# Performance work log

Hardware: AMD Instinct MI355X
Metric: run time of the kernel (lower is better)

## Reference

```python
import jax, jax.numpy as jnp
import numpy as np
import math

# ---- config (matches init_kwargs / Mamba defaults) ----
B_SZ = 16
IMG = 224
PATCH = 16
D_MODEL = 384
DEPTH = 24
D_INNER = 2 * D_MODEL          # expand=2
D_STATE = 16
D_CONV = 4
DT_RANK = math.ceil(D_MODEL / D_STATE)
N_CLASSES = 1000
L_TOK = (IMG // PATCH) ** 2     # 196

C_CURV = 0.5
SQRT_C = math.sqrt(C_CURV)
MAX_NORM = 0.95 / SQRT_C

# ---- StablePoincareBall ops ----
def _norm(x):
    return jnp.sqrt(jnp.sum(x * x, axis=-1, keepdims=True) + 1e-15)

def expmap0(u):
    n = jnp.clip(_norm(u), 1e-8, 5.0)
    res = jnp.tanh(SQRT_C * n) / SQRT_C * (u / n)
    rn = _norm(res)
    scale = jnp.where(rn > MAX_NORM, MAX_NORM / rn, jnp.ones_like(rn))
    return res * scale

def logmap0(y):
    n = jnp.clip(_norm(y), 1e-8, MAX_NORM)
    return jnp.arctanh(jnp.minimum(SQRT_C * n, 0.95)) / SQRT_C * (y / n)

def mobius_add(a, b):
    xy = jnp.sum(a * b, -1, keepdims=True)
    x2 = jnp.sum(a * a, -1, keepdims=True)
    y2 = jnp.sum(b * b, -1, keepdims=True)
    num = (1 + 2 * C_CURV * xy + C_CURV * y2) * a + (1 - C_CURV * x2) * b
    den = 1 + 2 * C_CURV * xy + (C_CURV ** 2) * x2 * y2
    return num / jnp.maximum(den, 1e-15)

def mobius_matvec(M, x):
    xn = jnp.maximum(_norm(x), 1e-8)
    mx = x @ M.T
    mxn = jnp.maximum(_norm(mx), 1e-8)
    t = jnp.tanh(mxn / xn * jnp.arctanh(jnp.minimum(SQRT_C * xn, 1.0 - 1e-5)))
    return t * mx / (mxn * SQRT_C)

def hyp_layernorm(x, gamma, beta, eps=1e-5):
    t = logmap0(x)
    mean = t.mean(-1, keepdims=True)
    # torch .std() is unbiased (ddof=1)
    var = jnp.sum((t - mean) ** 2, -1, keepdims=True) / (t.shape[-1] - 1)
    tn = (t - mean) / (jnp.sqrt(var) + eps)
    return expmap0(tn * gamma + beta)

def silu(x):
    return x * jax.nn.sigmoid(x)

# ---- Mamba selective scan (recompute dA per step; carry only h) ----
def selective_scan(u, dt, A, Bm, Cm):
    # u, dt: (B,L,Din); A: (Din,N); Bm, Cm: (B,L,N)
    def step(h, inp):
        dt_t, B_t, C_t, u_t = inp              # (B,Din),(B,N),(B,N),(B,Din)
        dA = jnp.exp(dt_t[..., None] * A)      # (B,Din,N)
        h = dA * h + dt_t[..., None] * B_t[:, None, :] * u_t[..., None]
        y = jnp.sum(h * C_t[:, None, :], -1)   # (B,Din)
        return h, y
    h0 = jnp.zeros((u.shape[0], u.shape[2], A.shape[1]), u.dtype)
    _, ys = jax.lax.scan(step, h0, (dt.transpose(1, 0, 2), Bm.transpose(1, 0, 2),
                                    Cm.transpose(1, 0, 2), u.transpose(1, 0, 2)))
    return ys.transpose(1, 0, 2)               # (B,L,Din)

def mamba_mixer(x, in_w, cw, cb, xp_w, dt_w, dt_b, A_log, Dp, out_w):
    xz = x @ in_w.T                            # (B,L,2*Din)
    xc, z = xz[..., :D_INNER], xz[..., D_INNER:]
    xt = xc.transpose(0, 2, 1)                 # (B,Din,L)
    xpad = jnp.pad(xt, ((0, 0), (0, 0), (D_CONV - 1, 0)))
    L = xt.shape[-1]
    conv = sum(cw[:, k][None, :, None] * xpad[:, :, k:k + L] for k in range(D_CONV))
    conv = conv + cb[None, :, None]
    u = silu(conv.transpose(0, 2, 1))          # (B,L,Din)
    dbl = u @ xp_w.T                           # (B,L,dt_rank+2N)
    dt_r = dbl[..., :DT_RANK]
    Bm = dbl[..., DT_RANK:DT_RANK + D_STATE]
    Cm = dbl[..., DT_RANK + D_STATE:]
    dt = jax.nn.softplus(dt_r @ dt_w.T + dt_b)
    A = -jnp.exp(A_log)
    y = selective_scan(u, dt, A, Bm, Cm) + Dp * u
    y = y * silu(z)
    return y @ out_w.T


def setup_inputs() -> dict:
    key = jax.random.key(0)
    ks = jax.random.split(key, 24)
    f32 = jnp.float32
    inp = {}
    inp['x'] = jax.random.normal(ks[0], (B_SZ, 3, IMG, IMG), f32)
    inp['patch_w'] = jax.random.normal(ks[1], (D_MODEL, 3, PATCH, PATCH), f32) * 0.02
    inp['patch_b'] = jax.random.normal(ks[2], (D_MODEL,), f32) * 0.005
    inp['hyp_w'] = jax.random.normal(ks[3], (D_MODEL, D_MODEL), f32) * (1.0 / math.sqrt(D_MODEL))
    inp['hyp_b'] = jax.random.normal(ks[4], (D_MODEL,), f32) * 0.01
    inp['pe_gamma'] = jnp.ones((D_MODEL,), f32)
    inp['pe_beta'] = jnp.zeros((D_MODEL,), f32)
    inp['pos_embed'] = jax.random.normal(ks[5], (1, L_TOK, D_MODEL), f32) * 0.02
    inp['in_proj_w'] = jax.random.normal(ks[6], (DEPTH, 2 * D_INNER, D_MODEL), f32) * 0.02
    inp['conv_w'] = jax.random.normal(ks[7], (DEPTH, D_INNER, D_CONV), f32) * 0.1
    inp['conv_b'] = jnp.zeros((DEPTH, D_INNER), f32)
    inp['x_proj_w'] = jax.random.normal(ks[8], (DEPTH, DT_RANK + 2 * D_STATE, D_INNER), f32) * 0.02
    inp['dt_proj_w'] = jax.random.normal(ks[9], (DEPTH, D_INNER, DT_RANK), f32) * (1.0 / math.sqrt(DT_RANK))
    inp['dt_proj_b'] = jnp.log(jnp.expm1(jnp.full((DEPTH, D_INNER), 0.01, f32)))  # dt init ~0.01
    inp['A_log'] = jnp.tile(jnp.log(jnp.arange(1, D_STATE + 1, dtype=f32))[None, None, :], (DEPTH, D_INNER, 1))
    inp['Dp'] = jnp.ones((DEPTH, D_INNER), f32)
    inp['out_proj_w'] = jax.random.normal(ks[10], (DEPTH, D_MODEL, D_INNER), f32) * (0.02 / math.sqrt(DEPTH))
    inp['gamma'] = jnp.ones((DEPTH, D_MODEL), f32)
    inp['beta'] = jnp.zeros((DEPTH, D_MODEL), f32)
    inp['gamma_f'] = jnp.ones((D_MODEL,), f32)
    inp['beta_f'] = jnp.zeros((D_MODEL,), f32)
    inp['prototypes'] = expmap0(jax.random.normal(ks[11], (N_CLASSES, D_MODEL), f32) * 0.1)
    return inp


def reference(x, patch_w, patch_b, hyp_w, hyp_b, pe_gamma, pe_beta, pos_embed,
              in_proj_w, conv_w, conv_b, x_proj_w, dt_proj_w, dt_proj_b,
              A_log, Dp, out_proj_w, gamma, beta, gamma_f, beta_f, prototypes):
    # patch embed conv
    feat = jax.lax.conv_general_dilated(x, patch_w, (PATCH, PATCH), 'VALID',
                                        dimension_numbers=('NCHW', 'OIHW', 'NCHW'))
    feat = feat + patch_b[None, :, None, None]
    B, D, Hp, Wp = feat.shape
    tokens = feat.reshape(B, D, Hp * Wp).transpose(0, 2, 1)   # (B,L,D)
    h = expmap0(tokens)
    h = mobius_add(mobius_matvec(hyp_w, h), hyp_b)
    h = hyp_layernorm(h, pe_gamma, pe_beta)
    h = expmap0(logmap0(h) + pos_embed)                        # tangent-space pos add
    hidden, residual = h, None
    for i in range(DEPTH):
        residual = hidden if residual is None else hidden + residual
        hn = hyp_layernorm(residual, gamma[i], beta[i])
        hidden = mamba_mixer(hn, in_proj_w[i], conv_w[i], conv_b[i], x_proj_w[i],
                             dt_proj_w[i], dt_proj_b[i], A_log[i], Dp[i], out_proj_w[i])
    residual = hidden + residual
    hf = hyp_layernorm(residual, gamma_f, beta_f)
    pooled = expmap0(logmap0(hf).mean(axis=1))                 # tangent mean pool
    # hyperbolic distance head: logits = -dist(x, prototypes)
    diff = mobius_add(-pooled[:, None, :], prototypes[None])
    dn = jnp.minimum(SQRT_C * _norm(diff)[..., 0], 1.0 - 1e-5)
    return -(2.0 / SQRT_C) * jnp.arctanh(dn)                   # (B, num_classes)
```

## Files before the change

### kernel.cpp

```cpp
#include <hip/hip_runtime.h>
#include <hip/hip_bf16.h>
#include <math.h>

#define D_MODEL 384
#define D_INNER 768
#define D_STATE 16
#define DT_RANK 24
#define NXP 56
#define LTOK 196
#define BSZ 16
#define NROW 3136
#define NDEPTH 24
#define NCLS 1000

constexpr float kSqrtC   = 0.70710678118654752440f;
constexpr float kMaxNorm = 0.95f / 0.70710678118654752440f;

typedef unsigned short u16;
typedef short  bf16x8 __attribute__((ext_vector_type(8)));
typedef u16    u16x8  __attribute__((ext_vector_type(8)));
typedef float  f32x4  __attribute__((ext_vector_type(4)));

__device__ __forceinline__ float clampf(float x, float lo, float hi) {
  return fminf(fmaxf(x, lo), hi);
}

__device__ __forceinline__ u16 f2bf(float f) {
  union { float f; unsigned u; } v; v.f = f;
  return (u16)((v.u + 0x7FFFu + ((v.u >> 16) & 1u)) >> 16);
}
__device__ __forceinline__ float bf2f(u16 s) {
  union { unsigned u; float f; } v; v.u = ((unsigned)s) << 16;
  return v.f;
}

__device__ __forceinline__ float fsig(float x) {
  return __fdividef(1.f, 1.f + __expf(-x));
}
__device__ __forceinline__ float fsilu(float x) { return x * fsig(x); }
__device__ __forceinline__ float fsoftplus(float x) {
  return (x > 20.f) ? x : __logf(1.f + __expf(x));
}
__device__ __forceinline__ float ftanh(float x) {
  float e = __expf(2.f * x);
  return __fdividef(e - 1.f, e + 1.f);
}
__device__ __forceinline__ float fatanh(float x) {
  return 0.5f * __logf(__fdividef(1.f + x, 1.f - x));
}

__device__ __forceinline__ float waveSum(float v) {
#pragma unroll
  for (int o = 1; o < 64; o <<= 1) v += __shfl_xor(v, o, 64);
  return v;
}

__device__ __forceinline__ float blockSum128(float v, float* sm) {
#pragma unroll
  for (int o = 32; o > 0; o >>= 1) v += __shfl_down(v, o, 64);
  __syncthreads();
  if ((threadIdx.x & 63) == 0) sm[threadIdx.x >> 6] = v;
  __syncthreads();
  return sm[0] + sm[1];
}

__global__ __launch_bounds__(256) void k_cvt(const float* __restrict__ s,
                                             u16* __restrict__ d, int n4) {
  int i = blockIdx.x * 256 + threadIdx.x;
  if (i >= n4) return;
  float4 v = ((const float4*)s)[i];
  short4 o = {(short)f2bf(v.x), (short)f2bf(v.y), (short)f2bf(v.z),
              (short)f2bf(v.w)};
  *(short4*)&d[(size_t)i * 4] = o;
}

__global__ __launch_bounds__(256) void k_im2col(const float* __restrict__ x,
                                                u16* __restrict__ P) {
  size_t idx = (size_t)blockIdx.x * 256 + threadIdx.x;
  if (idx >= (size_t)NROW * 768) return;
  int k = (int)(idx % 768);
  int r = (int)(idx / 768);
  int b = r / LTOK, t = r % LTOK;
  int hp = t / 14, wp = t % 14;
  int c = k / 256, rem = k % 256, i = rem / 16, j = rem % 16;
  P[idx] = f2bf(
      x[(((size_t)(b * 3 + c) * 224) + hp * 16 + i) * 224 + wp * 16 + j]);
}

#define LDA 40
__global__ __launch_bounds__(256) void k_gemm_bb(
    const u16* __restrict__ A, const u16* __restrict__ W,
    const float* __restrict__ bias, void* __restrict__ Cn,
    void* __restrict__ Ct, int K, int lda, int ldc, int ldct, int Nv, int act,
    int obf, int obf_t) {
  __shared__ u16 As[64 * LDA];
  __shared__ u16 Ws[64 * LDA];
  const int tid = threadIdx.x;
  const int m0 = blockIdx.x * 64;
  const int n0 = blockIdx.y * 64;
  const int lane = tid & 63;
  const int wave = tid >> 6;
  const int wm = wave & 1, wn = wave >> 1;
  const int lm = lane & 15;
  const int quad = lane >> 4;
  const int srow = tid >> 2;
  const int sseg = tid & 3;

  f32x4 acc[2][2];
#pragma unroll
  for (int i = 0; i < 2; i++)
#pragma unroll
    for (int j = 0; j < 2; j++) acc[i][j] = (f32x4){0.f, 0.f, 0.f, 0.f};

  const u16* rowA = A + (size_t)(m0 + srow) * lda + sseg * 8;
  const int wrow = n0 + srow;
  const u16* rowW = W + (size_t)wrow * K + sseg * 8;
  const bool wvalid = wrow < Nv;

  for (int k0 = 0; k0 < K; k0 += 32) {
    u16x8 av = {0, 0, 0, 0, 0, 0, 0, 0}, wv = {0, 0, 0, 0, 0, 0, 0, 0};
    if (k0 + 32 <= K) {
      av = *(const u16x8*)(rowA + k0);
      if (wvalid) wv = *(const u16x8*)(rowW + k0);
    } else {
#pragma unroll
      for (int kk = 0; kk < 8; kk++) {
        int k = k0 + sseg * 8 + kk;
        if (k < K) {
          av[kk] = rowA[k0 + kk];
          if (wvalid) wv[kk] = rowW[k0 + kk];
        }
      }
    }
    __syncthreads();
    *(u16x8*)&As[srow * LDA + sseg * 8] = av;
    *(u16x8*)&Ws[srow * LDA + sseg * 8] = wv;
    __syncthreads();
    bf16x8 af[2], bfr[2];
#pragma unroll
    for (int i = 0; i < 2; i++) {
      af[i]  = *(bf16x8*)&As[(wm * 32 + i * 16 + lm) * LDA + quad * 8];
      bfr[i] = *(bf16x8*)&Ws[(wn * 32 + i * 16 + lm) * LDA + quad * 8];
    }
#pragma unroll
    for (int i = 0; i < 2; i++)
#pragma unroll
      for (int j = 0; j < 2; j++)
        acc[i][j] = __builtin_amdgcn_mfma_f32_16x16x32_bf16(af[i], bfr[j],
                                                            acc[i][j], 0, 0, 0);
  }
#pragma unroll
  for (int i = 0; i < 2; i++) {
#pragma unroll
    for (int j = 0; j < 2; j++) {
      int cg = n0 + wn * 32 + j * 16 + lm;
      if (cg >= Nv) continue;
      float bj = bias ? bias[cg] : 0.f;
      float o[4];
      int rgb = m0 + wm * 32 + i * 16 + quad * 4;
#pragma unroll
      for (int reg = 0; reg < 4; reg++) {
        float v = acc[i][j][reg] + bj;
        if (act == 1) v = fsoftplus(v);
        else if (act == 2 && cg >= 768) v = fsilu(v);
        o[reg] = v;
      }
      if (Cn) {
#pragma unroll
        for (int reg = 0; reg < 4; reg++) {
          if (obf) ((u16*)Cn)[(size_t)(rgb + reg) * ldc + cg] = f2bf(o[reg]);
          else ((float*)Cn)[(size_t)(rgb + reg) * ldc + cg] = o[reg];
        }
      }
      if (Ct) {
        if (obf_t) {
          short4 o4 = {(short)f2bf(o[0]), (short)f2bf(o[1]), (short)f2bf(o[2]),
                       (short)f2bf(o[3])};
          *(short4*)&((u16*)Ct)[(size_t)cg * ldct + rgb] = o4;
        } else {
          float4 o4 = {o[0], o[1], o[2], o[3]};
          *(float4*)&((float*)Ct)[(size_t)cg * ldct + rgb] = o4;
        }
      }
    }
  }
}

__global__ __launch_bounds__(256) void k_gemm_n128(
    const u16* __restrict__ A, const u16* __restrict__ W,
    const float* __restrict__ bias, void* __restrict__ Cn, int K, int lda,
    int ldc, int act, int obf) {
  __shared__ u16 As[64 * LDA];
  __shared__ u16 Ws[128 * LDA];
  const int tid = threadIdx.x;
  const int m0 = blockIdx.x * 64;
  const int n0 = blockIdx.y * 128;
  const int lane = tid & 63;
  const int w = tid >> 6;
  const int lm = lane & 15;
  const int quad = lane >> 4;
  const int srow = tid >> 2;
  const int sseg = tid & 3;
  const int wrow = tid >> 1;
  const int wseg = tid & 1;

  f32x4 acc[4][2];
#pragma unroll
  for (int i = 0; i < 4; i++)
#pragma unroll
    for (int j = 0; j < 2; j++) acc[i][j] = (f32x4){0.f, 0.f, 0.f, 0.f};

  const u16* rowA = A + (size_t)(m0 + srow) * lda + sseg * 8;
  const u16* rowW = W + (size_t)(n0 + wrow) * K + wseg * 16;

  for (int k0 = 0; k0 < K; k0 += 32) {
    u16x8 av = *(const u16x8*)(rowA + k0);
    u16x8 wv0 = *(const u16x8*)(rowW + k0);
    u16x8 wv1 = *(const u16x8*)(rowW + k0 + 8);
    __syncthreads();
    *(u16x8*)&As[srow * LDA + sseg * 8] = av;
    *(u16x8*)&Ws[wrow * LDA + wseg * 16] = wv0;
    *(u16x8*)&Ws[wrow * LDA + wseg * 16 + 8] = wv1;
    __syncthreads();
    bf16x8 af[4], bfr[2];
#pragma unroll
    for (int i = 0; i < 4; i++)
      af[i] = *(bf16x8*)&As[(i * 16 + lm) * LDA + quad * 8];
#pragma unroll
    for (int j = 0; j < 2; j++)
      bfr[j] = *(bf16x8*)&Ws[(w * 32 + j * 16 + lm) * LDA + quad * 8];
#pragma unroll
    for (int i = 0; i < 4; i++)
#pragma unroll
      for (int j = 0; j < 2; j++)
        acc[i][j] = __builtin_amdgcn_mfma_f32_16x16x32_bf16(af[i], bfr[j],
                                                            acc[i][j], 0, 0, 0);
  }
#pragma unroll
  for (int i = 0; i < 4; i++) {
#pragma unroll
    for (int j = 0; j < 2; j++) {
      int cg = n0 + w * 32 + j * 16 + lm;
      float bj = bias ? bias[cg] : 0.f;
      int rgb = m0 + i * 16 + quad * 4;
#pragma unroll
      for (int reg = 0; reg < 4; reg++) {
        float v = acc[i][j][reg] + bj;
        if (act == 1) v = fsoftplus(v);
        else if (act == 2 && cg >= 768) v = fsilu(v);
        if (obf) ((u16*)Cn)[(size_t)(rgb + reg) * ldc + cg] = f2bf(v);
        else ((float*)Cn)[(size_t)(rgb + reg) * ldc + cg] = v;
      }
    }
  }
}

__global__ __launch_bounds__(128) void k_stem_a(const float* __restrict__ tok,
                                                u16* __restrict__ hb,
                                                float* __restrict__ xn) {
  __shared__ float sm[2];
  const int r = blockIdx.x, tid = threadIdx.x;
  float v[3];
#pragma unroll
  for (int j = 0; j < 3; j++) v[j] = tok[(size_t)r * D_MODEL + tid + j * 128];
  float s = blockSum128(v[0] * v[0] + v[1] * v[1] + v[2] * v[2], sm);
  float n = sqrtf(s + 1e-15f);
  float nc = clampf(n, 1e-8f, 5.f);
  float ke = tanhf(kSqrtC * nc) / (kSqrtC * nc);
  float rn = sqrtf(ke * ke * s + 1e-15f);
  float sc = rn > kMaxNorm ? kMaxNorm / rn : 1.f;
  float kk = ke * sc;
#pragma unroll
  for (int j = 0; j < 3; j++)
    hb[(size_t)r * D_MODEL + tid + j * 128] = f2bf(kk * v[j]);
  if (tid == 0) xn[r] = fmaxf(sqrtf(kk * kk * s + 1e-15f), 1e-8f);
}

__global__ __launch_bounds__(128) void k_stem_b(
    const float* __restrict__ mx, const float* __restrict__ xn,
    const float* __restrict__ hyp_b, const float* __restrict__ pe_g,
    const float* __restrict__ pe_b, const float* __restrict__ pos,
    float* __restrict__ outh) {
  __shared__ float sm[2];
  const int r = blockIdx.x, tid = threadIdx.x;
  const int t = r % LTOK;
  float mv[3], bv[3];
  int dd[3];
#pragma unroll
  for (int j = 0; j < 3; j++) {
    dd[j] = tid + j * 128;
    mv[j] = mx[(size_t)r * D_MODEL + dd[j]];
    bv[j] = hyp_b[dd[j]];
  }
  float smx = blockSum128(mv[0] * mv[0] + mv[1] * mv[1] + mv[2] * mv[2], sm);
  float mxn = fmaxf(sqrtf(smx + 1e-15f), 1e-8f);
  float xnv = xn[r];
  float tt = tanhf(mxn / xnv * atanhf(fminf(kSqrtC * xnv, 1.f - 1e-5f)));
  float kres = tt / (mxn * kSqrtC);
  float res[3];
#pragma unroll
  for (int j = 0; j < 3; j++) res[j] = kres * mv[j];
  float xy = blockSum128(res[0] * bv[0] + res[1] * bv[1] + res[2] * bv[2], sm);
  float y2 = blockSum128(bv[0] * bv[0] + bv[1] * bv[1] + bv[2] * bv[2], sm);
  float x2 = kres * kres * smx;
  float al = 1.f + xy + 0.5f * y2;
  float be = 1.f - 0.5f * x2;
  float den = fmaxf(1.f + xy + 0.25f * x2 * y2, 1e-15f);
  float h1[3];
#pragma unroll
  for (int j = 0; j < 3; j++) h1[j] = (al * res[j] + be * bv[j]) / den;
  float s1 = blockSum128(h1[0] * h1[0] + h1[1] * h1[1] + h1[2] * h1[2], sm);
  float n1 = sqrtf(s1 + 1e-15f);
  float nc1 = clampf(n1, 1e-8f, kMaxNorm);
  float kl = atanhf(fminf(kSqrtC * nc1, 0.95f)) / (kSqrtC * nc1);
  float tl[3];
#pragma unroll
  for (int j = 0; j < 3; j++) tl[j] = kl * h1[j];
  float mean = blockSum128(tl[0] + tl[1] + tl[2], sm) * (1.f / 384.f);
  float dv = 0.f;
#pragma unroll
  for (int j = 0; j < 3; j++) { float d = tl[j] - mean; dv += d * d; }
  float var = blockSum128(dv, sm) * (1.f / 383.f);
  float inv = 1.f / (sqrtf(var) + 1e-5f);
  float g[3];
#pragma unroll
  for (int j = 0; j < 3; j++)
    g[j] = (tl[j] - mean) * inv * pe_g[dd[j]] + pe_b[dd[j]];
  float sg = blockSum128(g[0] * g[0] + g[1] * g[1] + g[2] * g[2], sm);
  float ng = sqrtf(sg + 1e-15f);
  float nc2 = clampf(ng, 1e-8f, 5.f);
  float ke = tanhf(kSqrtC * nc2) / (kSqrtC * nc2);
  float rn = sqrtf(ke * ke * sg + 1e-15f);
  float sc = rn > kMaxNorm ? kMaxNorm / rn : 1.f;
  float kk = ke * sc;
  float s2 = kk * kk * sg;
  float n3 = sqrtf(s2 + 1e-15f);
  float nc3 = clampf(n3, 1e-8f, kMaxNorm);
  float kl2 = atanhf(fminf(kSqrtC * nc3, 0.95f)) / (kSqrtC * nc3);
  float v[3];
#pragma unroll
  for (int j = 0; j < 3; j++)
    v[j] = kl2 * kk * g[j] + pos[(size_t)t * D_MODEL + dd[j]];
  float sv = blockSum128(v[0] * v[0] + v[1] * v[1] + v[2] * v[2], sm);
  float nv = sqrtf(sv + 1e-15f);
  float nc4 = clampf(nv, 1e-8f, 5.f);
  float ke2 = tanhf(kSqrtC * nc4) / (kSqrtC * nc4);
  float rn2 = sqrtf(ke2 * ke2 * sv + 1e-15f);
  float sc2 = rn2 > kMaxNorm ? kMaxNorm / rn2 : 1.f;
#pragma unroll
  for (int j = 0; j < 3; j++)
    outh[(size_t)r * D_MODEL + dd[j]] = ke2 * sc2 * v[j];
}

__global__ __launch_bounds__(256) void k_resln(
    const float* __restrict__ hid, const float* __restrict__ res_in,
    float* __restrict__ res_out, const float* __restrict__ g_,
    const float* __restrict__ b_, u16* __restrict__ out_bf,
    float* __restrict__ out_f, int first, int out_logmap) {
  const int lane = threadIdx.x & 63;
  const int r = blockIdx.x * 4 + (threadIdx.x >> 6);
  float v[6];
  int dd[6];
#pragma unroll
  for (int j = 0; j < 6; j++) {
    dd[j] = lane + j * 64;
    size_t idx = (size_t)r * D_MODEL + dd[j];
    v[j] = hid[idx] + (first ? 0.f : res_in[idx]);
    res_out[idx] = v[j];
  }
  float ss = 0.f;
#pragma unroll
  for (int j = 0; j < 6; j++) ss += v[j] * v[j];
  float s = waveSum(ss);
  float n = sqrtf(s + 1e-15f);
  float nc = clampf(n, 1e-8f, kMaxNorm);
  float kl = fatanh(fminf(kSqrtC * nc, 0.95f)) / (kSqrtC * nc);
  float t[6];
  float ts = 0.f;
#pragma unroll
  for (int j = 0; j < 6; j++) { t[j] = kl * v[j]; ts += t[j]; }
  float mean = waveSum(ts) * (1.f / 384.f);
  float dv = 0.f;
#pragma unroll
  for (int j = 0; j < 6; j++) { float d = t[j] - mean; dv += d * d; }
  float var = waveSum(dv) * (1.f / 383.f);
  float inv = 1.f / (sqrtf(var) + 1e-5f);
  float g[6];
  float gs = 0.f;
#pragma unroll
  for (int j = 0; j < 6; j++) {
    g[j] = (t[j] - mean) * inv * g_[dd[j]] + b_[dd[j]];
    gs += g[j] * g[j];
  }
  float sg = waveSum(gs);
  float ng = sqrtf(sg + 1e-15f);
  float nc2 = clampf(ng, 1e-8f, 5.f);
  float ke = ftanh(kSqrtC * nc2) / (kSqrtC * nc2);
  float rn = sqrtf(ke * ke * sg + 1e-15f);
  float sc = rn > kMaxNorm ? kMaxNorm / rn : 1.f;
  float kk = ke * sc;
  if (!out_logmap) {
#pragma unroll
    for (int j = 0; j < 6; j++)
      out_bf[(size_t)r * D_MODEL + dd[j]] = f2bf(kk * g[j]);
  } else {
    float s2 = kk * kk * sg;
    float n3 = sqrtf(s2 + 1e-15f);
    float nc3 = clampf(n3, 1e-8f, kMaxNorm);
    float kl2 = fatanh(fminf(kSqrtC * nc3, 0.95f)) / (kSqrtC * nc3);
#pragma unroll
    for (int j = 0; j < 6; j++)
      out_f[(size_t)r * D_MODEL + dd[j]] = kl2 * kk * g[j];
  }
}

__global__ __launch_bounds__(256) void k_convt(const u16* __restrict__ xz,
                                               const float* __restrict__ cw,
                                               const float* __restrict__ cb,
                                               u16* __restrict__ ut,
                                               u16* __restrict__ un) {
  __shared__ u16 sx[52][68];
  __shared__ u16 su2[49][68];
  const int d0 = blockIdx.x * 64;
  const int l0 = blockIdx.y * 49;
  const int b = blockIdx.z;
  const int t = threadIdx.x;
#pragma unroll
  for (int i = 0; i < 4; i++) {
    int idx = t + i * 256;
    if (idx < 832) {
      int row = idx >> 4, seg = idx & 15;
      int l = l0 - 3 + row;
      short4 v = {0, 0, 0, 0};
      if (l >= 0) {
        const u16* p = xz + (size_t)(b * LTOK + l) * (2 * D_INNER) + d0 + seg * 4;
        v = *(const short4*)p;
      }
      *(short4*)&sx[row][seg * 4] = v;
    }
  }
  __syncthreads();
  const int dl = t & 63, lg = t >> 6;
  const int d = d0 + dl;
  const float c0 = cw[d * 4], c1 = cw[d * 4 + 1], c2 = cw[d * 4 + 2],
              c3 = cw[d * 4 + 3];
  const float bb = cb[d];
  for (int l = lg; l < 49; l += 4) {
    float acc = bb;
    acc = fmaf(c0, bf2f(sx[l + 0][dl]), acc);
    acc = fmaf(c1, bf2f(sx[l + 1][dl]), acc);
    acc = fmaf(c2, bf2f(sx[l + 2][dl]), acc);
    acc = fmaf(c3, bf2f(sx[l + 3][dl]), acc);
    su2[l][dl] = f2bf(fsilu(acc));
  }
  __syncthreads();
#pragma unroll
  for (int i = 0; i < 13; i++) {
    int idx = t + i * 256;
    if (idx < 3136) {
      int d_ = idx / 49, l_ = idx % 49;
      ut[(size_t)(d0 + d_) * NROW + b * LTOK + l0 + l_] = su2[l_][d_];
    }
  }
#pragma unroll
  for (int i = 0; i < 13; i++) {
    int idx = t + i * 256;
    if (idx < 3136) {
      int l_ = idx >> 6, d_ = idx & 63;
      un[(size_t)(b * LTOK + l0 + l_) * D_INNER + d0 + d_] = su2[l_][d_];
    }
  }
}

__global__ __launch_bounds__(256) void k_pscan(
    const u16* __restrict__ ut, const float* __restrict__ dblt,
    const float* __restrict__ dt_w, const float* __restrict__ dt_bias,
    const float* __restrict__ A_log, const float* __restrict__ Dp,
    u16* __restrict__ yt) {
  __shared__ float sdt[4][196];
  __shared__ float su[4][196];
  __shared__ float sprod[16][197];
  const int d0 = blockIdx.x * 4, b = blockIdx.y;
  const int t = threadIdx.x;
  const size_t col0 = (size_t)b * LTOK;
  if (t < 196) {
    float r[DT_RANK];
#pragma unroll
    for (int k = 0; k < DT_RANK; k++)
      r[k] = dblt[(size_t)k * NROW + col0 + t];
#pragma unroll
    for (int g = 0; g < 4; g++) {
      const int d = d0 + g;
      float acc = dt_bias[d];
#pragma unroll
      for (int k = 0; k < DT_RANK; k++)
        acc = fmaf(r[k], dt_w[d * DT_RANK + k], acc);
      sdt[g][t] = fsoftplus(acc);
      su[g][t] = bf2f(ut[(size_t)d * NROW + col0 + t]);
    }
  }
  const int c = t & 15, n = t >> 4;
  const bool act = c < 14;
  float Breg[14], Creg[14];
  if (act) {
    const float2* Bp =
        (const float2*)(dblt + (size_t)(DT_RANK + n) * NROW + col0 + c * 14);
    const float2* Cp = (const float2*)(
        dblt + (size_t)(DT_RANK + D_STATE + n) * NROW + col0 + c * 14);
#pragma unroll
    for (int j = 0; j < 7; j++) {
      float2 bv = Bp[j], cv = Cp[j];
      Breg[2 * j] = bv.x; Breg[2 * j + 1] = bv.y;
      Creg[2 * j] = cv.x; Creg[2 * j + 1] = cv.y;
    }
  }
  __syncthreads();
  for (int g = 0; g < 4; g++) {
    const int d = d0 + g;
    const float a = -__expf(A_log[(size_t)d * D_STATE + n]);
    float dA[14], hh[14];
    float A = 1.f, Bc = 0.f;
    if (act) {
      float h = 0.f, p = 1.f;
#pragma unroll
      for (int j = 0; j < 14; j++) {
        int l = c * 14 + j;
        float dtv = sdt[g][l];
        float e = __expf(dtv * a);
        h = fmaf(e, h, dtv * Breg[j] * su[g][l]);
        dA[j] = e;
        hh[j] = h;
        p *= e;
      }
      A = p;
      Bc = h;
    }
#pragma unroll
    for (int off = 1; off < 16; off <<= 1) {
      float pA = __shfl_up(A, off, 16);
      float pB = __shfl_up(Bc, off, 16);
      if (c >= off) {
        Bc = fmaf(A, pB, Bc);
        A *= pA;
      }
    }
    float h0 = __shfl_up(Bc, 1, 16);
    if (c == 0) h0 = 0.f;
    if (act) {
      float p = 1.f;
#pragma unroll
      for (int j = 0; j < 14; j++) {
        p *= dA[j];
        sprod[n][c * 14 + j] = fmaf(p, h0, hh[j]) * Creg[j];
      }
    }
    __syncthreads();
    if (t < 196) {
      float y = 0.f;
#pragma unroll
      for (int nn = 0; nn < 16; nn++) y += sprod[nn][t];
      yt[(size_t)d * NROW + col0 + t] = f2bf(fmaf(Dp[d], su[g][t], y));
    }
    __syncthreads();
  }
}

__global__ __launch_bounds__(256) void k_trgate(const u16* __restrict__ yt,
                                                const u16* __restrict__ xz,
                                                u16* __restrict__ yf) {
  __shared__ u16 st[49][68];
  const int d0 = blockIdx.x * 64;
  const int l0 = blockIdx.y * 49;
  const int b = blockIdx.z;
  const int t = threadIdx.x;
#pragma unroll
  for (int i = 0; i < 13; i++) {
    int idx = t + i * 256;
    if (idx < 3136) {
      int d_ = idx / 49, l_ = idx % 49;
      st[l_][d_] = yt[(size_t)(d0 + d_) * NROW + b * LTOK + l0 + l_];
    }
  }
  __syncthreads();
#pragma unroll
  for (int i = 0; i < 13; i++) {
    int idx = t + i * 256;
    if (idx < 3136) {
      int l_ = idx >> 6, d_ = idx & 63;
      size_t r = (size_t)(b * LTOK + l0 + l_);
      float z = bf2f(xz[r * (2 * D_INNER) + D_INNER + d0 + d_]);
      yf[r * D_INNER + d0 + d_] = f2bf(bf2f(st[l_][d_]) * z);
    }
  }
}

__global__ __launch_bounds__(128) void k_pool1(const float* __restrict__ tl,
                                               float* __restrict__ partial) {
  const int b = blockIdx.x, g = blockIdx.y, tid = threadIdx.x;
  float m[3] = {0.f, 0.f, 0.f};
  for (int l = g * 14; l < (g + 1) * 14; l++) {
    size_t row = ((size_t)b * LTOK + l) * D_MODEL;
#pragma unroll
    for (int j = 0; j < 3; j++) m[j] += tl[row + tid + j * 128];
  }
#pragma unroll
  for (int j = 0; j < 3; j++)
    partial[((size_t)b * 14 + g) * D_MODEL + tid + j * 128] = m[j];
}

__global__ __launch_bounds__(128) void k_pool2(const float* __restrict__ partial,
                                               float* __restrict__ pooled,
                                               float* __restrict__ x2v) {
  __shared__ float sm[2];
  const int b = blockIdx.x, tid = threadIdx.x;
  float m[3] = {0.f, 0.f, 0.f};
  for (int g = 0; g < 14; g++) {
    size_t row = ((size_t)b * 14 + g) * D_MODEL;
#pragma unroll
    for (int j = 0; j < 3; j++) m[j] += partial[row + tid + j * 128];
  }
#pragma unroll
  for (int j = 0; j < 3; j++) m[j] *= (1.f / (float)LTOK);
  float s = blockSum128(m[0] * m[0] + m[1] * m[1] + m[2] * m[2], sm);
  float n = sqrtf(s + 1e-15f);
  float nc = clampf(n, 1e-8f, 5.f);
  float ke = tanhf(kSqrtC * nc) / (kSqrtC * nc);
  float rn = sqrtf(ke * ke * s + 1e-15f);
  float sc = rn > kMaxNorm ? kMaxNorm / rn : 1.f;
  float kk = ke * sc;
  float p[3];
#pragma unroll
  for (int j = 0; j < 3; j++) {
    p[j] = kk * m[j];
    pooled[(size_t)b * D_MODEL + tid + j * 128] = p[j];
  }
  float s2 = blockSum128(p[0] * p[0] + p[1] * p[1] + p[2] * p[2], sm);
  if (tid == 0) x2v[b] = s2;
}

__global__ __launch_bounds__(256) void k_head(const float* __restrict__ pooled,
                                              const float* __restrict__ protos,
                                              const float* __restrict__ x2v,
                                              float* __restrict__ out) {
  __shared__ float sp[D_MODEL];
  const int b = blockIdx.y;
  const int c = blockIdx.x * 256 + threadIdx.x;
  for (int j = threadIdx.x; j < D_MODEL; j += 256)
    sp[j] = pooled[(size_t)b * D_MODEL + j];
  __syncthreads();
  if (c >= NCLS) return;
  const float* pr = protos + (size_t)c * D_MODEL;
  float dotv = 0.f, y2 = 0.f;
  for (int k = 0; k < D_MODEL; k++) {
    float w = pr[k];
    dotv += sp[k] * w;
    y2 += w * w;
  }
  float x2 = x2v[b];
  float xy = -dotv;
  float al = 1.f + xy + 0.5f * y2;
  float be = 1.f - 0.5f * x2;
  float num2 = al * al * x2 + 2.f * al * be * xy + be * be * y2;
  float den = fmaxf(1.f + xy + 0.25f * x2 * y2, 1e-15f);
  float r2 = num2 / (den * den) + 1e-15f;
  float dn = fminf(kSqrtC * sqrtf(r2), 1.f - 1e-5f);
  out[(size_t)b * NCLS + c] = -(2.f / kSqrtC) * atanhf(dn);
}

extern "C" void kernel_launch(void* const* d_in, const int* in_sizes, int n_in,
                              void* d_out, int out_size, void* d_ws,
                              size_t ws_size, hipStream_t stream) {
  const float* x        = (const float*)d_in[0];
  const float* patch_w  = (const float*)d_in[1];
  const float* patch_b  = (const float*)d_in[2];
  const float* hyp_w    = (const float*)d_in[3];
  const float* hyp_b    = (const float*)d_in[4];
  const float* pe_gamma = (const float*)d_in[5];
  const float* pe_beta  = (const float*)d_in[6];
  const float* pos      = (const float*)d_in[7];
  const float* in_w     = (const float*)d_in[8];
  const float* conv_w   = (const float*)d_in[9];
  const float* conv_b   = (const float*)d_in[10];
  const float* xp_w     = (const float*)d_in[11];
  const float* dt_w     = (const float*)d_in[12];
  const float* dt_bias  = (const float*)d_in[13];
  const float* A_log    = (const float*)d_in[14];
  const float* Dp       = (const float*)d_in[15];
  const float* out_w    = (const float*)d_in[16];
  const float* gamma    = (const float*)d_in[17];
  const float* beta     = (const float*)d_in[18];
  const float* gamma_f  = (const float*)d_in[19];
  const float* beta_f   = (const float*)d_in[20];
  const float* protos   = (const float*)d_in[21];
  float* out = (float*)d_out;

  char* cur = (char*)d_ws;
  auto alloc = [&](size_t bytes) {
    char* p = cur;
    cur += (bytes + 255) & ~(size_t)255;
    return (void*)p;
  };
  float* hidden  = (float*)alloc((size_t)NROW * D_MODEL * 4);
  float* resid   = (float*)alloc((size_t)NROW * D_MODEL * 4);
  float* dblt    = (float*)alloc((size_t)64 * NROW * 4);
  float* fscr    = (float*)alloc((size_t)NROW * 768 * 4);
  float* xn      = (float*)alloc((size_t)NROW * 4);
  float* pooled  = (float*)alloc((size_t)BSZ * D_MODEL * 4);
  float* x2v     = (float*)alloc((size_t)BSZ * 4);
  float* partial = (float*)alloc((size_t)BSZ * 14 * D_MODEL * 4);
  u16* hn_bf  = (u16*)alloc((size_t)NROW * D_MODEL * 2);
  u16* xz_bf  = (u16*)alloc((size_t)NROW * 2 * D_INNER * 2);
  u16* ut     = (u16*)alloc((size_t)D_INNER * NROW * 2);
  u16* u_bf   = (u16*)alloc((size_t)NROW * D_INNER * 2);
  u16* yt     = (u16*)alloc((size_t)D_INNER * NROW * 2);
  u16* yf     = (u16*)alloc((size_t)NROW * D_INNER * 2);
  const size_t n_inw  = (size_t)NDEPTH * 2 * D_INNER * D_MODEL;
  const size_t n_outw = (size_t)NDEPTH * D_MODEL * D_INNER;
  const size_t n_xpw  = (size_t)NDEPTH * NXP * D_INNER;
  const size_t n_pw   = (size_t)D_MODEL * 768;
  const size_t n_hw   = (size_t)D_MODEL * D_MODEL;
  u16* in_wb  = (u16*)alloc(n_inw * 2);
  u16* out_wb = (u16*)alloc(n_outw * 2);
  u16* xp_wb  = (u16*)alloc(n_xpw * 2);
  u16* p_wb   = (u16*)alloc(n_pw * 2);
  u16* h_wb   = (u16*)alloc(n_hw * 2);
  u16* P_bf     = ut;
  float* tokens = fscr;
  float* mx     = fscr + (size_t)NROW * D_MODEL;
  float* hnf    = fscr;

  k_cvt<<<dim3((int)((n_inw / 4 + 255) / 256)), dim3(256), 0, stream>>>(
      in_w, in_wb, (int)(n_inw / 4));
  k_cvt<<<dim3((int)((n_outw / 4 + 255) / 256)), dim3(256), 0, stream>>>(
      out_w, out_wb, (int)(n_outw / 4));
  k_cvt<<<dim3((int)((n_xpw / 4 + 255) / 256)), dim3(256), 0, stream>>>(
      xp_w, xp_wb, (int)(n_xpw / 4));
  k_cvt<<<dim3((int)((n_pw / 4 + 255) / 256)), dim3(256), 0, stream>>>(
      patch_w, p_wb, (int)(n_pw / 4));
  k_cvt<<<dim3((int)((n_hw / 4 + 255) / 256)), dim3(256), 0, stream>>>(
      hyp_w, h_wb, (int)(n_hw / 4));

  k_im2col<<<dim3((NROW * 768) / 256), dim3(256), 0, stream>>>(x, P_bf);
  k_gemm_bb<<<dim3(NROW / 64, 6), dim3(256), 0, stream>>>(
      P_bf, p_wb, patch_b, tokens, nullptr, 768, 768, D_MODEL, 0, D_MODEL, 0,
      0, 0);
  k_stem_a<<<dim3(NROW), dim3(128), 0, stream>>>(tokens, hn_bf, xn);
  k_gemm_bb<<<dim3(NROW / 64, 6), dim3(256), 0, stream>>>(
      hn_bf, h_wb, nullptr, mx, nullptr, D_MODEL, D_MODEL, D_MODEL, 0, D_MODEL,
      0, 0, 0);
  k_stem_b<<<dim3(NROW), dim3(128), 0, stream>>>(mx, xn, hyp_b, pe_gamma,
                                                 pe_beta, pos, hidden);
  for (int i = 0; i < NDEPTH; i++) {
    k_resln<<<dim3(NROW / 4), dim3(256), 0, stream>>>(
        hidden, resid, resid, gamma + (size_t)i * D_MODEL,
        beta + (size_t)i * D_MODEL, hn_bf, nullptr, i == 0 ? 1 : 0, 0);
    k_gemm_n128<<<dim3(NROW / 64, (2 * D_INNER) / 128), dim3(256), 0, stream>>>(
        hn_bf, in_wb + (size_t)i * 2 * D_INNER * D_MODEL, nullptr, xz_bf,
        D_MODEL, D_MODEL, 2 * D_INNER, 2, 1);
    k_convt<<<dim3(12, 4, BSZ), dim3(256), 0, stream>>>(
        xz_bf, conv_w + (size_t)i * D_INNER * 4, conv_b + (size_t)i * D_INNER,
        ut, u_bf);
    k_gemm_bb<<<dim3(NROW / 64, 1), dim3(256), 0, stream>>>(
        u_bf, xp_wb + (size_t)i * NXP * D_INNER, nullptr, nullptr, dblt,
        D_INNER, D_INNER, 0, NROW, NXP, 0, 0, 0);
    k_pscan<<<dim3(D_INNER / 4, BSZ), dim3(256), 0, stream>>>(
        ut, dblt, dt_w + (size_t)i * D_INNER * DT_RANK,
        dt_bias + (size_t)i * D_INNER, A_log + (size_t)i * D_INNER * D_STATE,
        Dp + (size_t)i * D_INNER, yt);
    k_trgate<<<dim3(12, 4, BSZ), dim3(256), 0, stream>>>(yt, xz_bf, yf);
    k_gemm_bb<<<dim3(NROW / 64, 6), dim3(256), 0, stream>>>(
        yf, out_wb + (size_t)i * D_MODEL * D_INNER, nullptr, hidden, nullptr,
        D_INNER, D_INNER, D_MODEL, 0, D_MODEL, 0, 0, 0);
  }
  k_resln<<<dim3(NROW / 4), dim3(256), 0, stream>>>(
      hidden, resid, resid, gamma_f, beta_f, nullptr, hnf, 0, 1);
  k_pool1<<<dim3(BSZ, 14), dim3(128), 0, stream>>>(hnf, partial);
  k_pool2<<<dim3(BSZ), dim3(128), 0, stream>>>(partial, pooled, x2v);
  k_head<<<dim3((NCLS + 255) / 256, BSZ), dim3(256), 0, stream>>>(pooled,
                                                                  protos, x2v,
                                                                  out);
}
```

Baseline: 2.440 ms.

## Use direct global-to-LDS swizzled GEMM loads and fuse gating into scan

Both bf16 GEMM kernels now stage A and W tiles with global_load_lds 16-byte transfers straight into shared memory. The tiles use an XOR-swizzled 64-wide layout, and each pass covers 64 of K instead of 32. This removes the register round-trip and the padded-LDS stores, and halves the number of barrier pairs per K. The SiLU(z) gating multiply is moved into the selective-scan kernel, which writes the row-major gated output directly. That removes the separate transpose/gate kernel and the transposed yt buffer. In exchange, the GEMM drops its Nv and K-tail guards, so the x_proj call now reads W rows past its 56 valid rows (results discarded) and relies on K being a multiple of 64.

```diff
diff --git a/kernel.cpp b/kernel.cpp
--- a/kernel.cpp
+++ b/kernel.cpp
@@ -32,6 +32,12 @@
 __device__ __forceinline__ float bf2f(u16 s) {
   union { unsigned u; float f; } v; v.u = ((unsigned)s) << 16;
   return v.f;
+}
+
+__device__ __forceinline__ void gload16(const u16* g, u16* l) {
+  __builtin_amdgcn_global_load_lds(
+      (const __attribute__((address_space(1))) unsigned int*)g,
+      (__attribute__((address_space(3))) unsigned int*)l, 16, 0, 0);
 }
 
 __device__ __forceinline__ float fsig(float x) {
@@ -87,24 +93,25 @@
       x[(((size_t)(b * 3 + c) * 224) + hp * 16 + i) * 224 + wp * 16 + j]);
 }
 
-#define LDA 40
 __global__ __launch_bounds__(256) void k_gemm_bb(
     const u16* __restrict__ A, const u16* __restrict__ W,
     const float* __restrict__ bias, void* __restrict__ Cn,
     void* __restrict__ Ct, int K, int lda, int ldc, int ldct, int Nv, int act,
     int obf, int obf_t) {
-  __shared__ u16 As[64 * LDA];
-  __shared__ u16 Ws[64 * LDA];
+  __shared__ u16 As[64 * 64];
+  __shared__ u16 Ws[64 * 64];
   const int tid = threadIdx.x;
   const int m0 = blockIdx.x * 64;
   const int n0 = blockIdx.y * 64;
   const int lane = tid & 63;
-  const int wave = tid >> 6;
-  const int wm = wave & 1, wn = wave >> 1;
+  const int w = tid >> 6;
+  const int wm = w & 1, wn = w >> 1;
   const int lm = lane & 15;
   const int quad = lane >> 4;
-  const int srow = tid >> 2;
-  const int sseg = tid & 3;
+  const int r8 = lane >> 3;
+  const int t8 = lane & 7;
+  const int gsg = t8 ^ r8;
+  const int s = lm & 7;
 
   f32x4 acc[2][2];
 #pragma unroll
@@ -112,42 +119,34 @@
 #pragma unroll
     for (int j = 0; j < 2; j++) acc[i][j] = (f32x4){0.f, 0.f, 0.f, 0.f};
 
-  const u16* rowA = A + (size_t)(m0 + srow) * lda + sseg * 8;
-  const int wrow = n0 + srow;
-  const u16* rowW = W + (size_t)wrow * K + sseg * 8;
-  const bool wvalid = wrow < Nv;
-
-  for (int k0 = 0; k0 < K; k0 += 32) {
-    u16x8 av = {0, 0, 0, 0, 0, 0, 0, 0}, wv = {0, 0, 0, 0, 0, 0, 0, 0};
-    if (k0 + 32 <= K) {
-      av = *(const u16x8*)(rowA + k0);
-      if (wvalid) wv = *(const u16x8*)(rowW + k0);
-    } else {
-#pragma unroll
-      for (int kk = 0; kk < 8; kk++) {
-        int k = k0 + sseg * 8 + kk;
-        if (k < K) {
-          av[kk] = rowA[k0 + kk];
-          if (wvalid) wv[kk] = rowW[k0 + kk];
-        }
-      }
-    }
+  for (int k0 = 0; k0 < K; k0 += 64) {
     __syncthreads();
-    *(u16x8*)&As[srow * LDA + sseg * 8] = av;
-    *(u16x8*)&Ws[srow * LDA + sseg * 8] = wv;
+#pragma unroll
+    for (int cc = 0; cc < 2; cc++) {
+      const int c = 2 * w + cc;
+      const int row = c * 8 + r8;
+      gload16(A + (size_t)(m0 + row) * lda + k0 + gsg * 8,
+              (u16*)As + (size_t)c * 512);
+      gload16(W + (size_t)(n0 + row) * K + k0 + gsg * 8,
+              (u16*)Ws + (size_t)c * 512);
+    }
     __syncthreads();
-    bf16x8 af[2], bfr[2];
-#pragma unroll
-    for (int i = 0; i < 2; i++) {
-      af[i]  = *(bf16x8*)&As[(wm * 32 + i * 16 + lm) * LDA + quad * 8];
-      bfr[i] = *(bf16x8*)&Ws[(wn * 32 + i * 16 + lm) * LDA + quad * 8];
-    }
-#pragma unroll
-    for (int i = 0; i < 2; i++)
-#pragma unroll
-      for (int j = 0; j < 2; j++)
-        acc[i][j] = __builtin_amdgcn_mfma_f32_16x16x32_bf16(af[i], bfr[j],
-                                                            acc[i][j], 0, 0, 0);
+#pragma unroll
+    for (int h = 0; h < 2; h++) {
+      const int col = (((h << 2) + quad) ^ s) << 3;
+      bf16x8 af[2], bfr[2];
+#pragma unroll
+      for (int i = 0; i < 2; i++) {
+        af[i]  = *(bf16x8*)&As[(wm * 32 + i * 16 + lm) * 64 + col];
+        bfr[i] = *(bf16x8*)&Ws[(wn * 32 + i * 16 + lm) * 64 + col];
+      }
+#pragma unroll
+      for (int i = 0; i < 2; i++)
+#pragma unroll
+        for (int j = 0; j < 2; j++)
+          acc[i][j] = __builtin_amdgcn_mfma_f32_16x16x32_bf16(
+              af[i], bfr[j], acc[i][j], 0, 0, 0);
+    }
   }
 #pragma unroll
   for (int i = 0; i < 2; i++) {
@@ -190,8 +189,8 @@
     const u16* __restrict__ A, const u16* __restrict__ W,
     const float* __restrict__ bias, void* __restrict__ Cn, int K, int lda,
     int ldc, int act, int obf) {
-  __shared__ u16 As[64 * LDA];
-  __shared__ u16 Ws[128 * LDA];
+  __shared__ u16 As[64 * 64];
+  __shared__ u16 Ws[128 * 64];
   const int tid = threadIdx.x;
   const int m0 = blockIdx.x * 64;
   const int n0 = blockIdx.y * 128;
@@ -199,10 +198,10 @@
   const int w = tid >> 6;
   const int lm = lane & 15;
   const int quad = lane >> 4;
-  const int srow = tid >> 2;
-  const int sseg = tid & 3;
-  const int wrow = tid >> 1;
-  const int wseg = tid & 1;
+  const int r8 = lane >> 3;
+  const int t8 = lane & 7;
+  const int gsg = t8 ^ r8;
+  const int s = lm & 7;
 
   f32x4 acc[4][2];
 #pragma unroll
@@ -210,31 +209,38 @@
 #pragma unroll
     for (int j = 0; j < 2; j++) acc[i][j] = (f32x4){0.f, 0.f, 0.f, 0.f};
 
-  const u16* rowA = A + (size_t)(m0 + srow) * lda + sseg * 8;
-  const u16* rowW = W + (size_t)(n0 + wrow) * K + wseg * 16;
-
-  for (int k0 = 0; k0 < K; k0 += 32) {
-    u16x8 av = *(const u16x8*)(rowA + k0);
-    u16x8 wv0 = *(const u16x8*)(rowW + k0);
-    u16x8 wv1 = *(const u16x8*)(rowW + k0 + 8);
+  for (int k0 = 0; k0 < K; k0 += 64) {
     __syncthreads();
-    *(u16x8*)&As[srow * LDA + sseg * 8] = av;
-    *(u16x8*)&Ws[wrow * LDA + wseg * 16] = wv0;
-    *(u16x8*)&Ws[wrow * LDA + wseg * 16 + 8] = wv1;
+#pragma unroll
+    for (int cc = 0; cc < 2; cc++) {
+      const int c = 2 * w + cc;
+      gload16(A + (size_t)(m0 + c * 8 + r8) * lda + k0 + gsg * 8,
+              (u16*)As + (size_t)c * 512);
+    }
+#pragma unroll
+    for (int cc = 0; cc < 4; cc++) {
+      const int c = 4 * w + cc;
+      gload16(W + (size_t)(n0 + c * 8 + r8) * K + k0 + gsg * 8,
+              (u16*)Ws + (size_t)c * 512);
+    }
     __syncthreads();
-    bf16x8 af[4], bfr[2];
-#pragma unroll
-    for (int i = 0; i < 4; i++)
-      af[i] = *(bf16x8*)&As[(i * 16 + lm) * LDA + quad * 8];
-#pragma unroll
-    for (int j = 0; j < 2; j++)
-      bfr[j] = *(bf16x8*)&Ws[(w * 32 + j * 16 + lm) * LDA + quad * 8];
-#pragma unroll
-    for (int i = 0; i < 4; i++)
+#pragma unroll
+    for (int h = 0; h < 2; h++) {
+      const int col = (((h << 2) + quad) ^ s) << 3;
+      bf16x8 af[4], bfr[2];
+#pragma unroll
+      for (int i = 0; i < 4; i++)
+        af[i] = *(bf16x8*)&As[(i * 16 + lm) * 64 + col];
 #pragma unroll
       for (int j = 0; j < 2; j++)
-        acc[i][j] = __builtin_amdgcn_mfma_f32_16x16x32_bf16(af[i], bfr[j],
-                                                            acc[i][j], 0, 0, 0);
+        bfr[j] = *(bf16x8*)&Ws[(w * 32 + j * 16 + lm) * 64 + col];
+#pragma unroll
+      for (int i = 0; i < 4; i++)
+#pragma unroll
+        for (int j = 0; j < 2; j++)
+          acc[i][j] = __builtin_amdgcn_mfma_f32_16x16x32_bf16(
+              af[i], bfr[j], acc[i][j], 0, 0, 0);
+    }
   }
 #pragma unroll
   for (int i = 0; i < 4; i++) {
@@ -476,13 +482,14 @@
     const u16* __restrict__ ut, const float* __restrict__ dblt,
     const float* __restrict__ dt_w, const float* __restrict__ dt_bias,
     const float* __restrict__ A_log, const float* __restrict__ Dp,
-    u16* __restrict__ yt) {
+    const u16* __restrict__ xz, u16* __restrict__ yf) {
   __shared__ float sdt[4][196];
   __shared__ float su[4][196];
   __shared__ float sprod[16][197];
   const int d0 = blockIdx.x * 4, b = blockIdx.y;
   const int t = threadIdx.x;
   const size_t col0 = (size_t)b * LTOK;
+  short4 zq = {0, 0, 0, 0};
   if (t < 196) {
     float r[DT_RANK];
 #pragma unroll
@@ -498,6 +505,7 @@
       sdt[g][t] = fsoftplus(acc);
       su[g][t] = bf2f(ut[(size_t)d * NROW + col0 + t]);
     }
+    zq = *(const short4*)&xz[(col0 + t) * (2 * D_INNER) + D_INNER + d0];
   }
   const int c = t & 15, n = t >> 4;
   const bool act = c < 14;
@@ -515,6 +523,9 @@
     }
   }
   __syncthreads();
+  u16 og[4];
+  const u16 zz[4] = {(u16)zq.x, (u16)zq.y, (u16)zq.z, (u16)zq.w};
+#pragma unroll
   for (int g = 0; g < 4; g++) {
     const int d = d0 + g;
     const float a = -__expf(A_log[(size_t)d * D_STATE + n]);
@@ -559,38 +570,14 @@
       float y = 0.f;
 #pragma unroll
       for (int nn = 0; nn < 16; nn++) y += sprod[nn][t];
-      yt[(size_t)d * NROW + col0 + t] = f2bf(fmaf(Dp[d], su[g][t], y));
+      float yv = bf2f(f2bf(fmaf(Dp[d], su[g][t], y)));
+      og[g] = f2bf(yv * bf2f(zz[g]));
     }
     __syncthreads();
   }
-}
-
-__global__ __launch_bounds__(256) void k_trgate(const u16* __restrict__ yt,
-                                                const u16* __restrict__ xz,
-                                                u16* __restrict__ yf) {
-  __shared__ u16 st[49][68];
-  const int d0 = blockIdx.x * 64;
-  const int l0 = blockIdx.y * 49;
-  const int b = blockIdx.z;
-  const int t = threadIdx.x;
-#pragma unroll
-  for (int i = 0; i < 13; i++) {
-    int idx = t + i * 256;
-    if (idx < 3136) {
-      int d_ = idx / 49, l_ = idx % 49;
-      st[l_][d_] = yt[(size_t)(d0 + d_) * NROW + b * LTOK + l0 + l_];
-    }
-  }
-  __syncthreads();
-#pragma unroll
-  for (int i = 0; i < 13; i++) {
-    int idx = t + i * 256;
-    if (idx < 3136) {
-      int l_ = idx >> 6, d_ = idx & 63;
-      size_t r = (size_t)(b * LTOK + l0 + l_);
-      float z = bf2f(xz[r * (2 * D_INNER) + D_INNER + d0 + d_]);
-      yf[r * D_INNER + d0 + d_] = f2bf(bf2f(st[l_][d_]) * z);
-    }
+  if (t < 196) {
+    short4 o4 = {(short)og[0], (short)og[1], (short)og[2], (short)og[3]};
+    *(short4*)&yf[(col0 + t) * D_INNER + d0] = o4;
   }
 }
 
@@ -712,7 +699,6 @@
   u16* xz_bf  = (u16*)alloc((size_t)NROW * 2 * D_INNER * 2);
   u16* ut     = (u16*)alloc((size_t)D_INNER * NROW * 2);
   u16* u_bf   = (u16*)alloc((size_t)NROW * D_INNER * 2);
-  u16* yt     = (u16*)alloc((size_t)D_INNER * NROW * 2);
   u16* yf     = (u16*)alloc((size_t)NROW * D_INNER * 2);
   const size_t n_inw  = (size_t)NDEPTH * 2 * D_INNER * D_MODEL;
   const size_t n_outw = (size_t)NDEPTH * D_MODEL * D_INNER;
@@ -766,8 +752,7 @@
     k_pscan<<<dim3(D_INNER / 4, BSZ), dim3(256), 0, stream>>>(
         ut, dblt, dt_w + (size_t)i * D_INNER * DT_RANK,
         dt_bias + (size_t)i * D_INNER, A_log + (size_t)i * D_INNER * D_STATE,
-        Dp + (size_t)i * D_INNER, yt);
-    k_trgate<<<dim3(12, 4, BSZ), dim3(256), 0, stream>>>(yt, xz_bf, yf);
+        Dp + (size_t)i * D_INNER, xz_bf, yf);
     k_gemm_bb<<<dim3(NROW / 64, 6), dim3(256), 0, stream>>>(
         yf, out_wb + (size_t)i * D_MODEL * D_INNER, nullptr, hidden, nullptr,
         D_INNER, D_INNER, D_MODEL, 0, D_MODEL, 0, 0, 0);
```

Measured after the change: 2.211 ms. 9.4% less time.
